# Kernel tuning notes

Hardware: AMD Instinct MI355X
Metric: run time of the kernel (lower is better)

The kernel has to match this reference:

```python
import jax, jax.numpy as jnp
import numpy as np

NUM_HEADS = 8


def _ln(x, w, b, eps=1e-5):
    mu = x.mean(-1, keepdims=True)
    var = ((x - mu) ** 2).mean(-1, keepdims=True)
    return (x - mu) * jax.lax.rsqrt(var + eps) * w + b


def _qkv(x, w, H, d):
    # x: (n, l, C) -> q,k,v each (n, H, l, d)
    n, l, _ = x.shape
    qkv = (x @ w.T).reshape(n, l, 3, H, d)
    qkv = jnp.transpose(qkv, (2, 0, 3, 1, 4))
    return qkv[0], qkv[1], qkv[2]


def _qkv_head(x, w, d):
    # x: (n, H, l, d) -> q,k,v each (n, H, l, d); linear acts on head_dim
    n, H, l, _ = x.shape
    qkv = (x @ w.T).reshape(n, H, l, 3, d)
    qkv = jnp.transpose(qkv, (3, 0, 1, 2, 4))
    return qkv[0], qkv[1], qkv[2]


def _attn(q, k, v, scale):
    s = jax.nn.softmax(jnp.einsum('nhqd,nhkd->nhqk', q, k) * scale, axis=-1)
    return jnp.einsum('nhqk,nhkd->nhqd', s, v)


def setup_inputs() -> dict:
    key = jax.random.key(0)
    ks = jax.random.split(key, 10)
    B, N, C = 16, 4096, 512
    l = 64
    H, d = NUM_HEADS, C // NUM_HEADS
    return {
        'x': jax.random.normal(ks[0], (B, N, C), jnp.float32),
        'n3_w': jnp.ones((C,), jnp.float32),
        'n3_b': jnp.zeros((C,), jnp.float32),
        'n4_w': jnp.ones((C,), jnp.float32),
        'n4_b': jnp.zeros((C,), jnp.float32),
        'ln1_w': jax.random.normal(ks[1], (3 * C, C), jnp.float32) * 0.02,
        'ln2_w': jax.random.normal(ks[2], (3 * C, C), jnp.float32) * 0.02,
        'ln3_w': jax.random.normal(ks[3], (3 * d, d), jnp.float32) * 0.02,
        'ln4_w': jax.random.normal(ks[4], (3 * d, d), jnp.float32) * 0.02,
        'pos1': jax.random.normal(ks[5], (1, l, C), jnp.float32),
        'pos2': jax.random.normal(ks[6], (1, l, C), jnp.float32),
        'pos3': jax.random.normal(ks[7], (1, H, l, d), jnp.float32),
        'pos4': jax.random.normal(ks[8], (1, H, l, d), jnp.float32),
    }


def reference(x, n3_w, n3_b, n4_w, n4_b, ln1_w, ln2_w, ln3_w, ln4_w,
              pos1, pos2, pos3, pos4):
    B, N, C = x.shape
    l = int(np.sqrt(N))
    H = NUM_HEADS
    d = C // H
    scale = d ** -0.5

    # window (row) branch
    x_w = _ln(x, n3_w, n3_b).reshape(B * l, l, C) + pos1
    q, k, v = _qkv(x_w, ln1_w, H, d)
    x_ww = _attn(q, k, v, scale) + pos3                     # (B*l, H, l, d)
    xw_q, xw_k, xw_v = _qkv_head(x_ww, ln3_w, d)

    # height (column) branch: transpose the l x l grid
    x_h = _ln(x, n4_w, n4_b).reshape(B, l, l, C)
    x_h = jnp.swapaxes(x_h, 1, 2).reshape(B * l, l, C) + pos2
    q, k, v = _qkv(x_h, ln2_w, H, d)
    x_hh = _attn(q, k, v, scale) + pos4
    xh_q, xh_k, xh_v = _qkv_head(x_hh, ln4_w, d)

    # cross-attention between the two axial branches
    o1 = _attn(xh_q, xw_k, xw_v, scale)                     # (B*l, H, l, d)
    o1 = jnp.swapaxes(o1, 1, 2).reshape(B, l, l, C)
    o1 = jnp.swapaxes(o1, 1, 2)
    o2 = _attn(xw_q, xh_k, xh_v, scale)
    o2 = jnp.swapaxes(o2, 1, 2).reshape(B, l, l, C)

    out = (o1 + o2).reshape(B, N, C) + x
    return out
```

## Files before the change

kernel.cpp:

```cpp
#include <hip/hip_runtime.h>
#include <hip/hip_bf16.h>

typedef unsigned short u16;
typedef __attribute__((ext_vector_type(8))) short bf16x8;
typedef __attribute__((ext_vector_type(4))) short bf16x4;
typedef __attribute__((ext_vector_type(4))) float floatx4;
typedef __attribute__((ext_vector_type(4))) unsigned short u16x4;

__device__ __forceinline__ float b2f(u16 u) {
  unsigned int i = ((unsigned int)u) << 16;
  return __builtin_bit_cast(float, i);
}
__device__ __forceinline__ u16 f2b(float f) {
  __hip_bfloat16 h = __float2bfloat16(f);
  return __builtin_bit_cast(u16, h);
}
#define MFMA16(a, b, c) __builtin_amdgcn_mfma_f32_16x16x32_bf16((a), (b), (c), 0, 0, 0)
#define LGKM0() __asm__ volatile("s_waitcnt lgkmcnt(0)" ::: "memory")
#define VM0() __asm__ volatile("s_waitcnt vmcnt(0)" ::: "memory")
#define BAR() do { __asm__ volatile("" ::: "memory"); \
  __builtin_amdgcn_s_barrier(); \
  __asm__ volatile("" ::: "memory"); } while (0)

#if __has_builtin(__builtin_amdgcn_mfma_f32_16x16x16bf16_1k)
#define HAVE_MFMA_K16 1
#define MFMA16K16(a, b, c) __builtin_amdgcn_mfma_f32_16x16x16bf16_1k((a), (b), (c), 0, 0, 0)
#else
#define HAVE_MFMA_K16 0
#endif

__device__ __forceinline__ void gload_lds16(const u16* g, u16* l) {
  __builtin_amdgcn_global_load_lds(
      (const __attribute__((address_space(1))) void*)g,
      (__attribute__((address_space(3))) void*)l, 16, 0, 0);
}

__global__ __launch_bounds__(256) void cvt_kernel(const float* __restrict__ a,
                                                  u16* __restrict__ o, int n4) {
  int i = blockIdx.x * 256 + threadIdx.x;
  if (i < n4) {
    float4 v = ((const float4*)a)[i];
    u16x4 r;
    r.x = f2b(v.x); r.y = f2b(v.y); r.z = f2b(v.z); r.w = f2b(v.w);
    ((u16x4*)o)[i] = r;
  }
}

__global__ __launch_bounds__(256) void ln_pos_kernel(
    const float* __restrict__ x, const float* __restrict__ n3w, const float* __restrict__ n3b,
    const float* __restrict__ n4w, const float* __restrict__ n4b,
    const float* __restrict__ pos1, const float* __restrict__ pos2,
    u16* __restrict__ yW, u16* __restrict__ yH) {
  int wv = threadIdx.x >> 6, lane = threadIdx.x & 63;
  int token = blockIdx.x * 4 + wv;
  int b = token >> 12, r = (token >> 6) & 63, c = token & 63;
  const float4* xr = (const float4*)(x + (size_t)token * 512) + lane * 2;
  float4 x0 = xr[0], x1 = xr[1];
  float v[8] = {x0.x, x0.y, x0.z, x0.w, x1.x, x1.y, x1.z, x1.w};
  float s = 0.f, ss = 0.f;
#pragma unroll
  for (int j = 0; j < 8; j++) { s += v[j]; ss += v[j] * v[j]; }
#pragma unroll
  for (int off = 1; off < 64; off <<= 1) { s += __shfl_xor(s, off); ss += __shfl_xor(ss, off); }
  float mu = s * (1.0f / 512.0f);
  float var = ss * (1.0f / 512.0f) - mu * mu;
  float rs = rsqrtf(var + 1e-5f);
  int ch0 = lane * 8;
  float w3[8], b3[8], w4[8], b4[8], p1[8], p2[8];
  *(float4*)&w3[0] = *(const float4*)(n3w + ch0); *(float4*)&w3[4] = *(const float4*)(n3w + ch0 + 4);
  *(float4*)&b3[0] = *(const float4*)(n3b + ch0); *(float4*)&b3[4] = *(const float4*)(n3b + ch0 + 4);
  *(float4*)&w4[0] = *(const float4*)(n4w + ch0); *(float4*)&w4[4] = *(const float4*)(n4w + ch0 + 4);
  *(float4*)&b4[0] = *(const float4*)(n4b + ch0); *(float4*)&b4[4] = *(const float4*)(n4b + ch0 + 4);
  const float* p1p = pos1 + (size_t)c * 512 + ch0;
  const float* p2p = pos2 + (size_t)r * 512 + ch0;
  *(float4*)&p1[0] = *(const float4*)p1p; *(float4*)&p1[4] = *(const float4*)(p1p + 4);
  *(float4*)&p2[0] = *(const float4*)p2p; *(float4*)&p2[4] = *(const float4*)(p2p + 4);
  bf16x8 ow, oh;
#pragma unroll
  for (int j = 0; j < 8; j++) {
    float xn = (v[j] - mu) * rs;
    ow[j] = (short)f2b(xn * w3[j] + b3[j] + p1[j]);
    oh[j] = (short)f2b(xn * w4[j] + b4[j] + p2[j]);
  }
  *(bf16x8*)(yW + (size_t)token * 512 + ch0) = ow;
  size_t hrow = (size_t)b * 4096 + (size_t)c * 64 + r;
  *(bf16x8*)(yH + hrow * 512 + ch0) = oh;
}

__global__ __launch_bounds__(512, 1) void qkv_gemm_kernel(
    const u16* __restrict__ A0, const u16* __restrict__ A1,
    const u16* __restrict__ W0, const u16* __restrict__ W1,
    u16* __restrict__ Z0, u16* __restrict__ Z1) {
  const int K = 512, N = 1536, NT = 8;
  extern __shared__ u16 lds[];
  int br = blockIdx.z;
  const u16* A = br ? A1 : A0;
  const u16* W = br ? W1 : W0;
  u16* Z = br ? Z1 : Z0;
  int lin = blockIdx.y * 6 + blockIdx.x;
  int nl = (lin & 7) * 192 + (lin >> 3);
  int m0 = (nl / 6) * 256, n0 = (nl % 6) * 256;
  int tid = threadIdx.x, lane = tid & 63, wv = tid >> 6;
  int wm = wv >> 2, wn = wv & 3;
  int ml = lane & 15, quad = lane >> 4;
  int l8 = lane >> 3;
  int scol = ((lane & 7) ^ l8) << 3;

  floatx4 acc[8][4];
#pragma unroll
  for (int mi = 0; mi < 8; mi++)
#pragma unroll
    for (int n = 0; n < 4; n++) acc[mi][n] = (floatx4){0.f, 0.f, 0.f, 0.f};

  auto stA = [&](int kt, int ab, int q) {
    int row = (wv < 4) ? (q * 32 + wv * 8) : (128 + q * 32 + (wv - 4) * 8);
    gload_lds16(A + (size_t)(m0 + row + l8) * K + kt + scol,
                &lds[ab * 16384 + row * 64]);
  };
  auto stB = [&](int kt, int bb, int q) {
    int row = q * 64 + wv * 8;
    gload_lds16(W + (size_t)(n0 + row + l8) * K + kt + scol,
                &lds[32768 + bb * 16384 + row * 64]);
  };
  auto rdA = [&](int ab, int row, int sl) {
    return *(const bf16x8*)&lds[ab * 16384 + row * 64 + (((sl ^ (row & 7)) & 7) << 3)];
  };
  auto rdB = [&](int bb, int row, int sl) {
    return *(const bf16x8*)&lds[32768 + bb * 16384 + row * 64 + (((sl ^ (row & 7)) & 7) << 3)];
  };

#pragma unroll
  for (int q = 0; q < 4; q++) { stA(0, 0, q); stB(0, 0, q); }
#pragma unroll
  for (int q = 0; q < 3; q++) { stA(64, 1, q); stB(64, 1, q); }
  __asm__ volatile("s_waitcnt vmcnt(6)" ::: "memory");
  BAR();

  for (int t = 0; t < NT; ++t) {
    int b = t & 1;
    bf16x8 bfr[4][2];
    {
      bf16x8 af[2][2];
#pragma unroll
      for (int n = 0; n < 4; n++)
#pragma unroll
        for (int kh = 0; kh < 2; kh++)
          bfr[n][kh] = rdB(b, wn * 64 + n * 16 + ml, kh * 4 + quad);
#pragma unroll
      for (int mh = 0; mh < 2; mh++)
#pragma unroll
        for (int kh = 0; kh < 2; kh++)
          af[mh][kh] = rdA(b, wm * 128 + mh * 16 + ml, kh * 4 + quad);
      if (t + 1 < NT) { stA((t + 1) * 64, (t + 1) & 1, 3); stB((t + 1) * 64, (t + 1) & 1, 3); }
      BAR();
      __builtin_amdgcn_s_setprio(1);
#pragma unroll
      for (int mh = 0; mh < 2; mh++)
#pragma unroll
        for (int n = 0; n < 4; n++) {
          acc[mh][n] = MFMA16(af[mh][0], bfr[n][0], acc[mh][n]);
          acc[mh][n] = MFMA16(af[mh][1], bfr[n][1], acc[mh][n]);
        }
      __builtin_amdgcn_s_setprio(0);
      BAR();
    }
#pragma unroll
    for (int p = 1; p < 4; p++) {
      bf16x8 af[2][2];
#pragma unroll
      for (int mh = 0; mh < 2; mh++)
#pragma unroll
        for (int kh = 0; kh < 2; kh++)
          af[mh][kh] = rdA(b, wm * 128 + (p * 2 + mh) * 16 + ml, kh * 4 + quad);
      if (t + 2 < NT) { stA((t + 2) * 64, b, p - 1); stB((t + 2) * 64, b, p - 1); }
      BAR();
      __builtin_amdgcn_s_setprio(1);
#pragma unroll
      for (int mh = 0; mh < 2; mh++)
#pragma unroll
        for (int n = 0; n < 4; n++) {
          acc[p * 2 + mh][n] = MFMA16(af[mh][0], bfr[n][0], acc[p * 2 + mh][n]);
          acc[p * 2 + mh][n] = MFMA16(af[mh][1], bfr[n][1], acc[p * 2 + mh][n]);
        }
      __builtin_amdgcn_s_setprio(0);
      if (p < 3) BAR();
    }
    if (t + 2 < NT) { __asm__ volatile("s_waitcnt vmcnt(6)" ::: "memory"); }
    else            { __asm__ volatile("s_waitcnt vmcnt(0)" ::: "memory"); }
    BAR();
  }

  u16* wl = lds + wv * 2048;
#pragma unroll
  for (int mp = 0; mp < 4; mp++) {
#pragma unroll
    for (int mh = 0; mh < 2; mh++) {
      int mi = mp * 2 + mh;
#pragma unroll
      for (int n = 0; n < 4; n++)
#pragma unroll
        for (int r = 0; r < 4; r++)
          wl[(mh * 16 + quad * 4 + r) * 64 + n * 16 + ml] = f2b(acc[mi][n][r]);
    }
    LGKM0();
#pragma unroll
    for (int p2 = 0; p2 < 4; p2++) {
      int lrow = p2 * 8 + (lane >> 3);
      int col8 = (lane & 7) * 8;
      bf16x8 vv = *(const bf16x8*)&wl[lrow * 64 + col8];
      int rg = m0 + wm * 128 + mp * 32 + lrow;
      *(bf16x8*)&Z[(size_t)rg * N + n0 + wn * 64 + col8] = vv;
    }
    LGKM0();
  }
}

__device__ __forceinline__ void attn_core(bf16x8 aq0, bf16x8 aq1,
                                          const u16 (*Ks)[72], const u16 (*Vt)[72],
                                          u16 (*Psw)[72], int lane, floatx4 o[4]) {
  int ml = lane & 15, quad = lane >> 4;
  floatx4 s[4];
#pragma unroll
  for (int nt = 0; nt < 4; nt++) {
    floatx4 z = (floatx4){0.f, 0.f, 0.f, 0.f};
    bf16x8 k0 = *(const bf16x8*)&Ks[nt * 16 + ml][quad * 8];
    bf16x8 k1 = *(const bf16x8*)&Ks[nt * 16 + ml][32 + quad * 8];
    z = MFMA16(k0, aq0, z);
    z = MFMA16(k1, aq1, z);
    s[nt] = z;
  }
  float m = -1e30f;
#pragma unroll
  for (int nt = 0; nt < 4; nt++)
#pragma unroll
    for (int r = 0; r < 4; r++) m = fmaxf(m, s[nt][r]);
  m = fmaxf(m, __shfl_xor(m, 16));
  m = fmaxf(m, __shfl_xor(m, 32));
  float mh = -m * 0.125f;
  float su = 0.f;
#pragma unroll
  for (int nt = 0; nt < 4; nt++)
#pragma unroll
    for (int r = 0; r < 4; r++) {
      float p = __expf(__builtin_fmaf(s[nt][r], 0.125f, mh));
      s[nt][r] = p; su += p;
    }
  su += __shfl_xor(su, 16);
  su += __shfl_xor(su, 32);
  float inv = 1.0f / su;
#if HAVE_MFMA_K16
  bf16x4 pa[4];
#pragma unroll
  for (int nt = 0; nt < 4; nt++)
#pragma unroll
    for (int r = 0; r < 4; r++) pa[nt][r] = (short)f2b(s[nt][r] * inv);
#pragma unroll
  for (int et = 0; et < 4; et++) {
    floatx4 z = (floatx4){0.f, 0.f, 0.f, 0.f};
#pragma unroll
    for (int nt = 0; nt < 4; nt++) {
      bf16x4 bv = *(const bf16x4*)&Vt[et * 16 + ml][nt * 16 + quad * 4];
      z = MFMA16K16(pa[nt], bv, z);
    }
    o[et] = z;
  }
#else
#pragma unroll
  for (int nt = 0; nt < 4; nt++)
#pragma unroll
    for (int r = 0; r < 4; r++)
      Psw[ml][nt * 16 + quad * 4 + r] = f2b(s[nt][r] * inv);
  LGKM0();
  bf16x8 ap0 = *(const bf16x8*)&Psw[ml][quad * 8];
  bf16x8 ap1 = *(const bf16x8*)&Psw[ml][32 + quad * 8];
#pragma unroll
  for (int et = 0; et < 4; et++) {
    floatx4 z = (floatx4){0.f, 0.f, 0.f, 0.f};
    bf16x8 b0 = *(const bf16x8*)&Vt[et * 16 + ml][quad * 8];
    bf16x8 b1 = *(const bf16x8*)&Vt[et * 16 + ml][32 + quad * 8];
    z = MFMA16(ap0, b0, z);
    z = MFMA16(ap1, b1, z);
    o[et] = z;
  }
#endif
}

__device__ __forceinline__ void head_qkv(const floatx4 o[4], const float* pp,
                                         const u16* lw, u16 (*Ks)[72], u16 (*Vt)[72],
                                         u16 (*Ps)[72], int wv, int lane,
                                         bf16x8& axq0, bf16x8& axq1) {
  int ml = lane & 15, quad = lane >> 4;
#pragma unroll
  for (int et = 0; et < 4; et++)
#pragma unroll
    for (int r = 0; r < 4; r++) {
      int qp = wv * 16 + quad * 4 + r, e = et * 16 + ml;
      Ps[quad * 4 + r][et * 16 + ml] = f2b(o[et][r] + pp[(size_t)qp * 64 + e]);
    }
  LGKM0();
  bf16x8 ax0 = *(const bf16x8*)&Ps[ml][quad * 8];
  bf16x8 ax1 = *(const bf16x8*)&Ps[ml][32 + quad * 8];
  LGKM0();
  __builtin_amdgcn_sched_barrier(0);
#pragma unroll
  for (int nj = 0; nj < 4; nj++) {
    int col = 64 + nj * 16 + ml;
    bf16x8 b0 = *(const bf16x8*)(lw + (size_t)col * 64 + quad * 8);
    bf16x8 b1 = *(const bf16x8*)(lw + (size_t)col * 64 + 32 + quad * 8);
    floatx4 z = (floatx4){0.f, 0.f, 0.f, 0.f};
    z = MFMA16(ax0, b0, z);
    z = MFMA16(ax1, b1, z);
#pragma unroll
    for (int r = 0; r < 4; r++)
      Ks[wv * 16 + quad * 4 + r][nj * 16 + ml] = f2b(z[r]);
  }
#pragma unroll
  for (int nj = 0; nj < 4; nj++) {
    int col = 128 + nj * 16 + ml;
    bf16x8 b0 = *(const bf16x8*)(lw + (size_t)col * 64 + quad * 8);
    bf16x8 b1 = *(const bf16x8*)(lw + (size_t)col * 64 + 32 + quad * 8);
    floatx4 z = (floatx4){0.f, 0.f, 0.f, 0.f};
    z = MFMA16(ax0, b0, z);
    z = MFMA16(ax1, b1, z);
#pragma unroll
    for (int r = 0; r < 4; r++)
      Vt[nj * 16 + ml][wv * 16 + quad * 4 + r] = f2b(z[r]);
  }
#pragma unroll
  for (int nj = 0; nj < 4; nj++) {
    int col = nj * 16 + ml;
    bf16x8 b0 = *(const bf16x8*)(lw + (size_t)col * 64 + quad * 8);
    bf16x8 b1 = *(const bf16x8*)(lw + (size_t)col * 64 + 32 + quad * 8);
    floatx4 z = (floatx4){0.f, 0.f, 0.f, 0.f};
    z = MFMA16(ax0, b0, z);
    z = MFMA16(ax1, b1, z);
#pragma unroll
    for (int r = 0; r < 4; r++)
      Ps[quad * 4 + r][nj * 16 + ml] = f2b(z[r]);
  }
  LGKM0();
  __builtin_amdgcn_sched_barrier(0);
  axq0 = *(const bf16x8*)&Ps[ml][quad * 8];
  axq1 = *(const bf16x8*)&Ps[ml][32 + quad * 8];
  LGKM0();
}

__global__ __launch_bounds__(256) void fused_attn_kernel(
    const u16* __restrict__ Zw, const u16* __restrict__ Zh,
    const u16* __restrict__ l3b, const u16* __restrict__ l4b,
    const float* __restrict__ pos3, const float* __restrict__ pos4,
    u16* __restrict__ o1b, u16* __restrict__ o2b) {
  int w = blockIdx.x, h = blockIdx.y;
  __shared__ u16 pool[23040];
  u16 (*KsW)[72] = (u16(*)[72])pool;
  u16 (*VtW)[72] = (u16(*)[72])(pool + 4608);
  u16 (*KsH)[72] = (u16(*)[72])(pool + 9216);
  u16 (*VtH)[72] = (u16(*)[72])(pool + 13824);
  int tid = threadIdx.x, lane = tid & 63, wv = tid >> 6;
  int ml = lane & 15, quad = lane >> 4;
  u16 (*Ps)[72] = (u16(*)[72])(pool + 18432 + wv * 1152);
  const u16* baseW = Zw + (size_t)w * 64 * 1536 + h * 64;
  const u16* baseH = Zh + (size_t)w * 64 * 1536 + h * 64;
  for (int i = tid; i < 512; i += 256) {
    int r = i >> 3, c = (i & 7) * 8;
    *(bf16x8*)&KsW[r][c] = *(const bf16x8*)(baseW + 512 + (size_t)r * 1536 + c);
    *(bf16x8*)&KsH[r][c] = *(const bf16x8*)(baseH + 512 + (size_t)r * 1536 + c);
  }
  {
    int pg = tid & 15, eg = tid >> 4;
    u16x4 a0[4], a1[4];
#pragma unroll
    for (int j = 0; j < 4; j++) {
      a0[j] = *(const u16x4*)(baseW + 1024 + (size_t)(4 * pg + j) * 1536 + 4 * eg);
      a1[j] = *(const u16x4*)(baseH + 1024 + (size_t)(4 * pg + j) * 1536 + 4 * eg);
    }
#pragma unroll
    for (int k2 = 0; k2 < 4; k2++) {
      u16x4 w0 = {(u16)a0[0][k2], (u16)a0[1][k2], (u16)a0[2][k2], (u16)a0[3][k2]};
      u16x4 w1 = {(u16)a1[0][k2], (u16)a1[1][k2], (u16)a1[2][k2], (u16)a1[3][k2]};
      *(u16x4*)&VtW[4 * eg + k2][4 * pg] = w0;
      *(u16x4*)&VtH[4 * eg + k2][4 * pg] = w1;
    }
  }
  const u16* qrW = baseW + (size_t)(wv * 16 + ml) * 1536 + quad * 8;
  const u16* qrH = baseH + (size_t)(wv * 16 + ml) * 1536 + quad * 8;
  bf16x8 aqW0 = *(const bf16x8*)qrW;
  bf16x8 aqW1 = *(const bf16x8*)(qrW + 32);
  bf16x8 aqH0 = *(const bf16x8*)qrH;
  bf16x8 aqH1 = *(const bf16x8*)(qrH + 32);
  __syncthreads();
  floatx4 oW[4], oH[4];
  attn_core(aqW0, aqW1, KsW, VtW, Ps, lane, oW);
  attn_core(aqH0, aqH1, KsH, VtH, Ps, lane, oH);
  __syncthreads();
  bf16x8 axqW0, axqW1, axqH0, axqH1;
  head_qkv(oW, pos3 + (size_t)h * 4096, l3b, KsW, VtW, Ps, wv, lane, axqW0, axqW1);
  head_qkv(oH, pos4 + (size_t)h * 4096, l4b, KsH, VtH, Ps, wv, lane, axqH0, axqH1);
  __syncthreads();
  floatx4 c2[4], c1[4];
  attn_core(axqW0, axqW1, KsH, VtH, Ps, lane, c2);
  attn_core(axqH0, axqH1, KsW, VtW, Ps, lane, c1);
  __syncthreads();
  u16 (*Out1)[72] = (u16(*)[72])pool;
  u16 (*Out2)[72] = (u16(*)[72])(pool + 4608);
#pragma unroll
  for (int et = 0; et < 4; et++)
#pragma unroll
    for (int r = 0; r < 4; r++) {
      int row = wv * 16 + quad * 4 + r;
      Out1[row][et * 16 + ml] = f2b(c1[et][r]);
      Out2[row][et * 16 + ml] = f2b(c2[et][r]);
    }
  __syncthreads();
  u16* o1p = o1b + (size_t)w * 32768 + h * 64;
  u16* o2p = o2b + (size_t)w * 32768 + h * 64;
#pragma unroll
  for (int j = 0; j < 2; j++) {
    int c = tid + j * 256;
    int pos = c >> 3, cc = (c & 7) * 8;
    *(bf16x8*)&o1p[(size_t)pos * 512 + cc] = *(const bf16x8*)&Out1[pos][cc];
    *(bf16x8*)&o2p[(size_t)pos * 512 + cc] = *(const bf16x8*)&Out2[pos][cc];
  }
}

__global__ __launch_bounds__(256) void final_add_kernel(
    const float* __restrict__ x, const u16* __restrict__ o1b,
    const u16* __restrict__ o2b, float* __restrict__ out) {
  int wv = threadIdx.x >> 6, lane = threadIdx.x & 63;
  int token = blockIdx.x * 4 + wv;
  int b = token >> 12, r = (token >> 6) & 63, c = token & 63;
  size_t i = (size_t)token * 512 + lane * 8;
  size_t i1 = ((size_t)b * 4096 + (size_t)c * 64 + r) * 512 + lane * 8;
  float vx[8];
  *(float4*)&vx[0] = *(const float4*)(x + i);
  *(float4*)&vx[4] = *(const float4*)(x + i + 4);
  bf16x8 v1 = *(const bf16x8*)(o1b + i1);
  bf16x8 v2 = *(const bf16x8*)(o2b + i);
  float vo[8];
#pragma unroll
  for (int j = 0; j < 8; j++)
    vo[j] = vx[j] + b2f((u16)v1[j]) + b2f((u16)v2[j]);
  *(float4*)(out + i) = *(float4*)&vo[0];
  *(float4*)(out + i + 4) = *(float4*)&vo[4];
}

extern "C" void kernel_launch(void* const* d_in, const int* in_sizes, int n_in,
                              void* d_out, int out_size, void* d_ws, size_t ws_size,
                              hipStream_t stream) {
  const float* x    = (const float*)d_in[0];
  const float* n3w  = (const float*)d_in[1];
  const float* n3b  = (const float*)d_in[2];
  const float* n4w  = (const float*)d_in[3];
  const float* n4b  = (const float*)d_in[4];
  const float* ln1  = (const float*)d_in[5];
  const float* ln2  = (const float*)d_in[6];
  const float* ln3  = (const float*)d_in[7];
  const float* ln4  = (const float*)d_in[8];
  const float* pos1 = (const float*)d_in[9];
  const float* pos2 = (const float*)d_in[10];
  const float* pos3 = (const float*)d_in[11];
  const float* pos4 = (const float*)d_in[12];

  char* ws = (char*)d_ws;
  u16* yW = (u16*)ws;
  u16* yH = (u16*)(ws + (size_t)67108864);
  u16* Zw = (u16*)(ws + (size_t)134217728);
  u16* Zh = (u16*)(ws + (size_t)335544320);
  u16* o1b = yW;
  u16* o2b = yH;
  float* out = (float*)d_out;

  u16* Wb1 = (u16*)d_out;
  u16* Wb2 = Wb1 + 786432;
  u16* l3b = Wb2 + 786432;
  u16* l4b = l3b + 12288;

  static bool lds_attr_set = false;
  if (!lds_attr_set) {
    hipFuncSetAttribute((const void*)qkv_gemm_kernel,
                        hipFuncAttributeMaxDynamicSharedMemorySize, 131072);
    lds_attr_set = true;
  }

  cvt_kernel<<<768, 256, 0, stream>>>(ln1, Wb1, 196608);
  cvt_kernel<<<768, 256, 0, stream>>>(ln2, Wb2, 196608);
  cvt_kernel<<<12, 256, 0, stream>>>(ln3, l3b, 3072);
  cvt_kernel<<<12, 256, 0, stream>>>(ln4, l4b, 3072);
  ln_pos_kernel<<<16384, 256, 0, stream>>>(x, n3w, n3b, n4w, n4b, pos1, pos2, yW, yH);
  qkv_gemm_kernel<<<dim3(6, 256, 2), 512, 131072, stream>>>(yW, yH, Wb1, Wb2, Zw, Zh);
  fused_attn_kernel<<<dim3(1024, 8), 256, 0, stream>>>(Zw, Zh, l3b, l4b, pos3, pos4, o1b, o2b);
  final_add_kernel<<<16384, 256, 0, stream>>>(x, o1b, o2b, out);
}
```

Baseline: 836.2 us.

## Keep attention intermediates in transposed MFMA register layout, drop LDS staging

Swaps MFMA operand order so outputs come out transposed, letting the softmax probabilities, head-level QKV projection input and cross-attention queries stay in registers as bf16x4 fragments instead of round-tripping through a per-wave LDS scratch buffer. The per-wave Ps scratch is removed, shrinking shared memory, and pos-embedding loads plus output writes are vectorized. This removes LDS writes, reads and waits in the head projection and attention stages, at the cost of more k16 MFMAs and a fallback inline-asm path.

```diff
diff --git a/kernel.cpp b/kernel.cpp
--- a/kernel.cpp
+++ b/kernel.cpp
@@ -23,10 +23,16 @@
   __asm__ volatile("" ::: "memory"); } while (0)
 
 #if __has_builtin(__builtin_amdgcn_mfma_f32_16x16x16bf16_1k)
-#define HAVE_MFMA_K16 1
-#define MFMA16K16(a, b, c) __builtin_amdgcn_mfma_f32_16x16x16bf16_1k((a), (b), (c), 0, 0, 0)
+__device__ __forceinline__ floatx4 mfma_k16(bf16x4 a, bf16x4 b, floatx4 c) {
+  return __builtin_amdgcn_mfma_f32_16x16x16bf16_1k(a, b, c, 0, 0, 0);
+}
 #else
-#define HAVE_MFMA_K16 0
+__device__ __forceinline__ floatx4 mfma_k16(bf16x4 a, bf16x4 b, floatx4 c) {
+  floatx4 d;
+  __asm__("v_mfma_f32_16x16x16_bf16 %0, %1, %2, %3"
+          : "=v"(d) : "v"(a), "v"(b), "v"(c));
+  return d;
+}
 #endif
 
 __device__ __forceinline__ void gload_lds16(const u16* g, u16* l) {
@@ -215,9 +221,35 @@
   }
 }
 
-__device__ __forceinline__ void attn_core(bf16x8 aq0, bf16x8 aq1,
-                                          const u16 (*Ks)[72], const u16 (*Vt)[72],
-                                          u16 (*Psw)[72], int lane, floatx4 o[4]) {
+__device__ __forceinline__ void softmax_pa(floatx4 s[4], bf16x4 pa[4]) {
+  float m = -1e30f;
+#pragma unroll
+  for (int nt = 0; nt < 4; nt++)
+#pragma unroll
+    for (int r = 0; r < 4; r++) m = fmaxf(m, s[nt][r]);
+  m = fmaxf(m, __shfl_xor(m, 16));
+  m = fmaxf(m, __shfl_xor(m, 32));
+  float mh = -m * 0.125f;
+  float su = 0.f;
+#pragma unroll
+  for (int nt = 0; nt < 4; nt++)
+#pragma unroll
+    for (int r = 0; r < 4; r++) {
+      float p = __expf(__builtin_fmaf(s[nt][r], 0.125f, mh));
+      s[nt][r] = p; su += p;
+    }
+  su += __shfl_xor(su, 16);
+  su += __shfl_xor(su, 32);
+  float inv = 1.0f / su;
+#pragma unroll
+  for (int nt = 0; nt < 4; nt++)
+#pragma unroll
+    for (int r = 0; r < 4; r++) pa[nt][r] = (short)f2b(s[nt][r] * inv);
+}
+
+__device__ __forceinline__ void attn_window(bf16x8 aq0, bf16x8 aq1,
+                                            const u16 (*Ks)[72], const u16 (*Vt)[72],
+                                            int lane, floatx4 o[4]) {
   int ml = lane & 15, quad = lane >> 4;
   floatx4 s[4];
 #pragma unroll
@@ -229,120 +261,97 @@
     z = MFMA16(k1, aq1, z);
     s[nt] = z;
   }
-  float m = -1e30f;
-#pragma unroll
-  for (int nt = 0; nt < 4; nt++)
-#pragma unroll
-    for (int r = 0; r < 4; r++) m = fmaxf(m, s[nt][r]);
-  m = fmaxf(m, __shfl_xor(m, 16));
-  m = fmaxf(m, __shfl_xor(m, 32));
-  float mh = -m * 0.125f;
-  float su = 0.f;
-#pragma unroll
-  for (int nt = 0; nt < 4; nt++)
-#pragma unroll
-    for (int r = 0; r < 4; r++) {
-      float p = __expf(__builtin_fmaf(s[nt][r], 0.125f, mh));
-      s[nt][r] = p; su += p;
-    }
-  su += __shfl_xor(su, 16);
-  su += __shfl_xor(su, 32);
-  float inv = 1.0f / su;
-#if HAVE_MFMA_K16
   bf16x4 pa[4];
-#pragma unroll
-  for (int nt = 0; nt < 4; nt++)
-#pragma unroll
-    for (int r = 0; r < 4; r++) pa[nt][r] = (short)f2b(s[nt][r] * inv);
+  softmax_pa(s, pa);
 #pragma unroll
   for (int et = 0; et < 4; et++) {
     floatx4 z = (floatx4){0.f, 0.f, 0.f, 0.f};
 #pragma unroll
     for (int nt = 0; nt < 4; nt++) {
       bf16x4 bv = *(const bf16x4*)&Vt[et * 16 + ml][nt * 16 + quad * 4];
-      z = MFMA16K16(pa[nt], bv, z);
+      z = mfma_k16(bv, pa[nt], z);
     }
     o[et] = z;
   }
-#else
-#pragma unroll
-  for (int nt = 0; nt < 4; nt++)
-#pragma unroll
-    for (int r = 0; r < 4; r++)
-      Psw[ml][nt * 16 + quad * 4 + r] = f2b(s[nt][r] * inv);
-  LGKM0();
-  bf16x8 ap0 = *(const bf16x8*)&Psw[ml][quad * 8];
-  bf16x8 ap1 = *(const bf16x8*)&Psw[ml][32 + quad * 8];
+}
+
+__device__ __forceinline__ void attn_cross(const bf16x4 axq[4],
+                                           const u16 (*Ks)[72], const u16 (*Vt)[72],
+                                           int lane, floatx4 o[4]) {
+  int ml = lane & 15, quad = lane >> 4;
+  floatx4 s[4];
+#pragma unroll
+  for (int pt = 0; pt < 4; pt++) {
+    floatx4 z = (floatx4){0.f, 0.f, 0.f, 0.f};
+#pragma unroll
+    for (int nt = 0; nt < 4; nt++) {
+      bf16x4 ka = *(const bf16x4*)&Ks[pt * 16 + ml][nt * 16 + quad * 4];
+      z = mfma_k16(ka, axq[nt], z);
+    }
+    s[pt] = z;
+  }
+  bf16x4 pa[4];
+  softmax_pa(s, pa);
 #pragma unroll
   for (int et = 0; et < 4; et++) {
     floatx4 z = (floatx4){0.f, 0.f, 0.f, 0.f};
-    bf16x8 b0 = *(const bf16x8*)&Vt[et * 16 + ml][quad * 8];
-    bf16x8 b1 = *(const bf16x8*)&Vt[et * 16 + ml][32 + quad * 8];
-    z = MFMA16(ap0, b0, z);
-    z = MFMA16(ap1, b1, z);
+#pragma unroll
+    for (int nt = 0; nt < 4; nt++) {
+      bf16x4 bv = *(const bf16x4*)&Vt[et * 16 + ml][nt * 16 + quad * 4];
+      z = mfma_k16(bv, pa[nt], z);
+    }
     o[et] = z;
   }
-#endif
 }
 
 __device__ __forceinline__ void head_qkv(const floatx4 o[4], const float* pp,
                                          const u16* lw, u16 (*Ks)[72], u16 (*Vt)[72],
-                                         u16 (*Ps)[72], int wv, int lane,
-                                         bf16x8& axq0, bf16x8& axq1) {
+                                         int wv, int lane, bf16x4 axq[4]) {
   int ml = lane & 15, quad = lane >> 4;
-#pragma unroll
-  for (int et = 0; et < 4; et++)
-#pragma unroll
-    for (int r = 0; r < 4; r++) {
-      int qp = wv * 16 + quad * 4 + r, e = et * 16 + ml;
-      Ps[quad * 4 + r][et * 16 + ml] = f2b(o[et][r] + pp[(size_t)qp * 64 + e]);
-    }
-  LGKM0();
-  bf16x8 ax0 = *(const bf16x8*)&Ps[ml][quad * 8];
-  bf16x8 ax1 = *(const bf16x8*)&Ps[ml][32 + quad * 8];
-  LGKM0();
-  __builtin_amdgcn_sched_barrier(0);
-#pragma unroll
-  for (int nj = 0; nj < 4; nj++) {
-    int col = 64 + nj * 16 + ml;
-    bf16x8 b0 = *(const bf16x8*)(lw + (size_t)col * 64 + quad * 8);
-    bf16x8 b1 = *(const bf16x8*)(lw + (size_t)col * 64 + 32 + quad * 8);
-    floatx4 z = (floatx4){0.f, 0.f, 0.f, 0.f};
-    z = MFMA16(ax0, b0, z);
-    z = MFMA16(ax1, b1, z);
+  bf16x4 x[4];
+#pragma unroll
+  for (int et = 0; et < 4; et++) {
+    float4 pv = *(const float4*)&pp[(size_t)(wv * 16 + ml) * 64 + et * 16 + quad * 4];
+    float pvv[4] = {pv.x, pv.y, pv.z, pv.w};
+#pragma unroll
+    for (int r = 0; r < 4; r++) x[et][r] = (short)f2b(o[et][r] + pvv[r]);
+  }
+#pragma unroll
+  for (int n2 = 0; n2 < 4; n2++) {
+    floatx4 z = (floatx4){0.f, 0.f, 0.f, 0.f};
+#pragma unroll
+    for (int nt = 0; nt < 4; nt++) {
+      bf16x4 la = *(const bf16x4*)(lw + (size_t)(n2 * 16 + ml) * 64 + nt * 16 + quad * 4);
+      z = mfma_k16(la, x[nt], z);
+    }
+#pragma unroll
+    for (int r = 0; r < 4; r++) axq[n2][r] = (short)f2b(z[r]);
+  }
+#pragma unroll
+  for (int n2 = 0; n2 < 4; n2++) {
+    floatx4 z = (floatx4){0.f, 0.f, 0.f, 0.f};
+#pragma unroll
+    for (int nt = 0; nt < 4; nt++) {
+      bf16x4 la = *(const bf16x4*)(lw + (size_t)(64 + n2 * 16 + ml) * 64 + nt * 16 + quad * 4);
+      z = mfma_k16(la, x[nt], z);
+    }
+    u16x4 kv;
+#pragma unroll
+    for (int r = 0; r < 4; r++) kv[r] = f2b(z[r]);
+    *(u16x4*)&Ks[wv * 16 + ml][n2 * 16 + quad * 4] = kv;
+  }
+#pragma unroll
+  for (int n2 = 0; n2 < 4; n2++) {
+    floatx4 z = (floatx4){0.f, 0.f, 0.f, 0.f};
+#pragma unroll
+    for (int nt = 0; nt < 4; nt++) {
+      bf16x4 la = *(const bf16x4*)(lw + (size_t)(128 + n2 * 16 + ml) * 64 + nt * 16 + quad * 4);
+      z = mfma_k16(la, x[nt], z);
+    }
 #pragma unroll
     for (int r = 0; r < 4; r++)
-      Ks[wv * 16 + quad * 4 + r][nj * 16 + ml] = f2b(z[r]);
-  }
-#pragma unroll
-  for (int nj = 0; nj < 4; nj++) {
-    int col = 128 + nj * 16 + ml;
-    bf16x8 b0 = *(const bf16x8*)(lw + (size_t)col * 64 + quad * 8);
-    bf16x8 b1 = *(const bf16x8*)(lw + (size_t)col * 64 + 32 + quad * 8);
-    floatx4 z = (floatx4){0.f, 0.f, 0.f, 0.f};
-    z = MFMA16(ax0, b0, z);
-    z = MFMA16(ax1, b1, z);
-#pragma unroll
-    for (int r = 0; r < 4; r++)
-      Vt[nj * 16 + ml][wv * 16 + quad * 4 + r] = f2b(z[r]);
-  }
-#pragma unroll
-  for (int nj = 0; nj < 4; nj++) {
-    int col = nj * 16 + ml;
-    bf16x8 b0 = *(const bf16x8*)(lw + (size_t)col * 64 + quad * 8);
-    bf16x8 b1 = *(const bf16x8*)(lw + (size_t)col * 64 + 32 + quad * 8);
-    floatx4 z = (floatx4){0.f, 0.f, 0.f, 0.f};
-    z = MFMA16(ax0, b0, z);
-    z = MFMA16(ax1, b1, z);
-#pragma unroll
-    for (int r = 0; r < 4; r++)
-      Ps[quad * 4 + r][nj * 16 + ml] = f2b(z[r]);
-  }
-  LGKM0();
-  __builtin_amdgcn_sched_barrier(0);
-  axq0 = *(const bf16x8*)&Ps[ml][quad * 8];
-  axq1 = *(const bf16x8*)&Ps[ml][32 + quad * 8];
-  LGKM0();
+      Vt[n2 * 16 + quad * 4 + r][wv * 16 + ml] = f2b(z[r]);
+  }
 }
 
 __global__ __launch_bounds__(256) void fused_attn_kernel(
@@ -351,14 +360,13 @@
     const float* __restrict__ pos3, const float* __restrict__ pos4,
     u16* __restrict__ o1b, u16* __restrict__ o2b) {
   int w = blockIdx.x, h = blockIdx.y;
-  __shared__ u16 pool[23040];
+  __shared__ u16 pool[18432];
   u16 (*KsW)[72] = (u16(*)[72])pool;
   u16 (*VtW)[72] = (u16(*)[72])(pool + 4608);
   u16 (*KsH)[72] = (u16(*)[72])(pool + 9216);
   u16 (*VtH)[72] = (u16(*)[72])(pool + 13824);
   int tid = threadIdx.x, lane = tid & 63, wv = tid >> 6;
   int ml = lane & 15, quad = lane >> 4;
-  u16 (*Ps)[72] = (u16(*)[72])(pool + 18432 + wv * 1152);
   const u16* baseW = Zw + (size_t)w * 64 * 1536 + h * 64;
   const u16* baseH = Zh + (size_t)w * 64 * 1536 + h * 64;
   for (int i = tid; i < 512; i += 256) {
@@ -390,27 +398,27 @@
   bf16x8 aqH1 = *(const bf16x8*)(qrH + 32);
   __syncthreads();
   floatx4 oW[4], oH[4];
-  attn_core(aqW0, aqW1, KsW, VtW, Ps, lane, oW);
-  attn_core(aqH0, aqH1, KsH, VtH, Ps, lane, oH);
+  attn_window(aqW0, aqW1, KsW, VtW, lane, oW);
+  attn_window(aqH0, aqH1, KsH, VtH, lane, oH);
   __syncthreads();
-  bf16x8 axqW0, axqW1, axqH0, axqH1;
-  head_qkv(oW, pos3 + (size_t)h * 4096, l3b, KsW, VtW, Ps, wv, lane, axqW0, axqW1);
-  head_qkv(oH, pos4 + (size_t)h * 4096, l4b, KsH, VtH, Ps, wv, lane, axqH0, axqH1);
+  bf16x4 axqW[4], axqH[4];
+  head_qkv(oW, pos3 + (size_t)h * 4096, l3b, KsW, VtW, wv, lane, axqW);
+  head_qkv(oH, pos4 + (size_t)h * 4096, l4b, KsH, VtH, wv, lane, axqH);
   __syncthreads();
   floatx4 c2[4], c1[4];
-  attn_core(axqW0, axqW1, KsH, VtH, Ps, lane, c2);
-  attn_core(axqH0, axqH1, KsW, VtW, Ps, lane, c1);
+  attn_cross(axqW, KsH, VtH, lane, c2);
+  attn_cross(axqH, KsW, VtW, lane, c1);
   __syncthreads();
   u16 (*Out1)[72] = (u16(*)[72])pool;
   u16 (*Out2)[72] = (u16(*)[72])(pool + 4608);
 #pragma unroll
-  for (int et = 0; et < 4; et++)
-#pragma unroll
-    for (int r = 0; r < 4; r++) {
-      int row = wv * 16 + quad * 4 + r;
-      Out1[row][et * 16 + ml] = f2b(c1[et][r]);
-      Out2[row][et * 16 + ml] = f2b(c2[et][r]);
-    }
+  for (int et = 0; et < 4; et++) {
+    u16x4 v1, v2;
+#pragma unroll
+    for (int r = 0; r < 4; r++) { v1[r] = f2b(c1[et][r]); v2[r] = f2b(c2[et][r]); }
+    *(u16x4*)&Out1[wv * 16 + ml][et * 16 + quad * 4] = v1;
+    *(u16x4*)&Out2[wv * 16 + ml][et * 16 + quad * 4] = v2;
+  }
   __syncthreads();
   u16* o1p = o1b + (size_t)w * 32768 + h * 64;
   u16* o2p = o2b + (size_t)w * 32768 + h * 64;
```

Result: slower. 1.035 ms (+23.8%).
